# Optimization experiments

Hardware: AMD Instinct MI355X
Metric: run time of the kernel (lower is better)

## Reference

```python
import jax, jax.numpy as jnp
import numpy as np

K = 3  # spatial window (window_size = [1,3,3,1])


def _extract_patches(x, k):
    """TF-style extract_patches, VALID padding, stride 1, rate 1.
    x: [B,H,W,C] -> [B,Ho,Wo,k*k*C] with depth ordering (ki, kj, c)."""
    B, H, W, C = x.shape
    Ho, Wo = H - k + 1, W - k + 1
    cols = [x[:, ki:ki + Ho, kj:kj + Wo, :] for ki in range(k) for kj in range(k)]
    return jnp.concatenate(cols, axis=-1)


def setup_inputs() -> dict:
    key = jax.random.key(0)
    k1, k2 = jax.random.split(key)
    x = jax.random.normal(k1, (8, 32, 32, 32), dtype=jnp.float32)
    # weight shape per build(): (1, 1, 1, K*K*C, filters) = (1,1,1,288,64)
    w = jax.random.normal(k2, (1, 1, 1, 3 * 3 * 32, 64), dtype=jnp.float32) * 0.05
    bias = jnp.zeros((64,), dtype=jnp.float32)
    return {"x": x, "w": w, "bias": bias}


def reference(x, w, bias):
    # patches: [B,Ho,Wo,KKC]
    p = _extract_patches(x, K)
    # broadcast add: [B,Ho,Wo,KKC,1] + [KKC,F] -> [B,Ho,Wo,KKC,F]
    r = p[..., None] + w[0, 0, 0]
    # tropical conv: max-plus minus min-plus over the patch axis, plus bias
    return jnp.max(r, axis=3) - jnp.min(r, axis=3) + bias
```

## Files before the change

kernel.cpp:

```cpp
#include <hip/hip_runtime.h>
#include <math.h>


#define NCOL 10

__global__ __launch_bounds__(256) void trop_kernel(
    const float* __restrict__ x, const float* __restrict__ w,
    const float* __restrict__ bias, float* __restrict__ out) {
  __shared__ float wl[96 * 64];
  __shared__ float xt[3 * 32 * NCOL];

  const int jg = blockIdx.x;
  const int i = blockIdx.y;
  const int b = blockIdx.z;
  const int tid = threadIdx.x;
  const int f = tid & 63;
  const int wave = tid >> 6;
  const int jw = wave * 2;
  const int j0 = jg * 8;

  const float* xb = x + (((size_t)b * 32 + i) * 32) * 32;
  if (tid < 240) {
    int ki = tid / 80;
    int rem = tid % 80;
    int col = rem / 8;
    int c4 = (rem % 8) * 4;
    if (j0 + col < 32) {
      float4 v = *(const float4*)(xb + ((size_t)(ki * 32 + j0 + col)) * 32 + c4);
      xt[(ki * 32 + c4 + 0) * NCOL + col] = v.x;
      xt[(ki * 32 + c4 + 1) * NCOL + col] = v.y;
      xt[(ki * 32 + c4 + 2) * NCOL + col] = v.z;
      xt[(ki * 32 + c4 + 3) * NCOL + col] = v.w;
    }
  }

  float mx0 = -INFINITY, mx1 = -INFINITY;
  float mn0 = INFINITY, mn1 = INFINITY;

  for (int ki = 0; ki < 3; ++ki) {
    __syncthreads();
    const float4* wg = (const float4*)(w + ki * 96 * 64);
    float4* wld = (float4*)wl;
#pragma unroll
    for (int t = 0; t < 6; ++t) wld[tid + t * 256] = wg[tid + t * 256];
    __syncthreads();

#pragma unroll
    for (int c = 0; c < 32; ++c) {
      const float* row = &xt[(ki * 32 + c) * NCOL];
      float2 a = *(const float2*)(row + jw);
      float2 d = *(const float2*)(row + jw + 2);
      float w0 = wl[(0 * 32 + c) * 64 + f];
      float w1 = wl[(1 * 32 + c) * 64 + f];
      float w2 = wl[(2 * 32 + c) * 64 + f];
      float t00 = a.x + w0, t01 = a.y + w0;
      float t10 = a.y + w1, t11 = d.x + w1;
      float t20 = d.x + w2, t21 = d.y + w2;
      mx0 = fmaxf(mx0, fmaxf(t00, fmaxf(t10, t20)));
      mx1 = fmaxf(mx1, fmaxf(t01, fmaxf(t11, t21)));
      mn0 = fminf(mn0, fminf(t00, fminf(t10, t20)));
      mn1 = fminf(mn1, fminf(t01, fminf(t11, t21)));
    }
  }

  float bv = bias[f];
  float* ob = out + (((size_t)b * 30 + i) * 30) * 64 + f;
  int j = j0 + jw;
  if (j < 30) ob[(size_t)j * 64] = mx0 - mn0 + bv;
  if (j + 1 < 30) ob[(size_t)(j + 1) * 64] = mx1 - mn1 + bv;
}

extern "C" void kernel_launch(void* const* d_in, const int* in_sizes, int n_in,
                              void* d_out, int out_size, void* d_ws, size_t ws_size,
                              hipStream_t stream) {
  const float* x = (const float*)d_in[0];
  const float* w = (const float*)d_in[1];
  const float* bias = (const float*)d_in[2];
  float* out = (float*)d_out;
  dim3 grid(4, 30, 8);
  dim3 block(256);
  hipLaunchKernelGGL(trop_kernel, grid, block, 0, stream, x, w, bias, out);
}
```

Baseline: 71.78 us.

## Compute four output columns per thread with direct wave-uniform input loads

Drops the LDS staging of the input tile and has each wave read its six input columns straight from global memory. The column offset is made wave-uniform with readfirstlane, so those loads can become scalar loads. Each thread now produces four output columns instead of two, and the grid's column dimension shrinks from 4 to 2 blocks. Each shared-memory weight element is therefore reused over more outputs, and the total weight staging traffic is halved. The two column groups overlap at columns 14-15, which are computed and written twice with identical values; fewer blocks also means less parallelism.

```diff
diff --git a/kernel.cpp b/kernel.cpp
--- a/kernel.cpp
+++ b/kernel.cpp
@@ -1,41 +1,22 @@
 #include <hip/hip_runtime.h>
 #include <math.h>
 
-
-#define NCOL 10
 
 __global__ __launch_bounds__(256) void trop_kernel(
     const float* __restrict__ x, const float* __restrict__ w,
     const float* __restrict__ bias, float* __restrict__ out) {
   __shared__ float wl[96 * 64];
-  __shared__ float xt[3 * 32 * NCOL];
 
   const int jg = blockIdx.x;
   const int i = blockIdx.y;
   const int b = blockIdx.z;
   const int tid = threadIdx.x;
   const int f = tid & 63;
-  const int wave = tid >> 6;
-  const int jw = wave * 2;
-  const int j0 = jg * 8;
+  const int jwu = __builtin_amdgcn_readfirstlane(tid >> 6) * 4;
+  const int j0 = jg * 14 + jwu;
 
-  const float* xb = x + (((size_t)b * 32 + i) * 32) * 32;
-  if (tid < 240) {
-    int ki = tid / 80;
-    int rem = tid % 80;
-    int col = rem / 8;
-    int c4 = (rem % 8) * 4;
-    if (j0 + col < 32) {
-      float4 v = *(const float4*)(xb + ((size_t)(ki * 32 + j0 + col)) * 32 + c4);
-      xt[(ki * 32 + c4 + 0) * NCOL + col] = v.x;
-      xt[(ki * 32 + c4 + 1) * NCOL + col] = v.y;
-      xt[(ki * 32 + c4 + 2) * NCOL + col] = v.z;
-      xt[(ki * 32 + c4 + 3) * NCOL + col] = v.w;
-    }
-  }
-
-  float mx0 = -INFINITY, mx1 = -INFINITY;
-  float mn0 = INFINITY, mn1 = INFINITY;
+  float mx[4] = {-INFINITY, -INFINITY, -INFINITY, -INFINITY};
+  float mn[4] = {INFINITY, INFINITY, INFINITY, INFINITY};
 
   for (int ki = 0; ki < 3; ++ki) {
     __syncthreads();
@@ -45,29 +26,42 @@
     for (int t = 0; t < 6; ++t) wld[tid + t * 256] = wg[tid + t * 256];
     __syncthreads();
 
+    const float* xr = x + (((size_t)b * 32 + (i + ki)) * 32 + j0) * 32;
+
 #pragma unroll
-    for (int c = 0; c < 32; ++c) {
-      const float* row = &xt[(ki * 32 + c) * NCOL];
-      float2 a = *(const float2*)(row + jw);
-      float2 d = *(const float2*)(row + jw + 2);
-      float w0 = wl[(0 * 32 + c) * 64 + f];
-      float w1 = wl[(1 * 32 + c) * 64 + f];
-      float w2 = wl[(2 * 32 + c) * 64 + f];
-      float t00 = a.x + w0, t01 = a.y + w0;
-      float t10 = a.y + w1, t11 = d.x + w1;
-      float t20 = d.x + w2, t21 = d.y + w2;
-      mx0 = fmaxf(mx0, fmaxf(t00, fmaxf(t10, t20)));
-      mx1 = fmaxf(mx1, fmaxf(t01, fmaxf(t11, t21)));
-      mn0 = fminf(mn0, fminf(t00, fminf(t10, t20)));
-      mn1 = fminf(mn1, fminf(t01, fminf(t11, t21)));
+    for (int c8 = 0; c8 < 32; c8 += 8) {
+      float4 xa[6][2];
+#pragma unroll
+      for (int col = 0; col < 6; ++col) {
+        xa[col][0] = *(const float4*)(xr + col * 32 + c8);
+        xa[col][1] = *(const float4*)(xr + col * 32 + c8 + 4);
+      }
+      const float* wbase = &wl[c8 * 64 + f];
+#pragma unroll
+      for (int c = 0; c < 8; ++c) {
+        float w0 = wbase[c * 64];
+        float w1 = wbase[32 * 64 + c * 64];
+        float w2 = wbase[64 * 64 + c * 64];
+        float xv[6];
+#pragma unroll
+        for (int col = 0; col < 6; ++col)
+          xv[col] = ((const float*)xa[col])[c];
+#pragma unroll
+        for (int p = 0; p < 4; ++p) {
+          float a0 = xv[p + 0] + w0;
+          float a1 = xv[p + 1] + w1;
+          float a2 = xv[p + 2] + w2;
+          mx[p] = fmaxf(mx[p], fmaxf(a0, fmaxf(a1, a2)));
+          mn[p] = fminf(mn[p], fminf(a0, fminf(a1, a2)));
+        }
+      }
     }
   }
 
   float bv = bias[f];
-  float* ob = out + (((size_t)b * 30 + i) * 30) * 64 + f;
-  int j = j0 + jw;
-  if (j < 30) ob[(size_t)j * 64] = mx0 - mn0 + bv;
-  if (j + 1 < 30) ob[(size_t)(j + 1) * 64] = mx1 - mn1 + bv;
+  float* ob = out + (((size_t)b * 30 + i) * 30 + j0) * 64 + f;
+#pragma unroll
+  for (int p = 0; p < 4; ++p) ob[p * 64] = mx[p] - mn[p] + bv;
 }
 
 extern "C" void kernel_launch(void* const* d_in, const int* in_sizes, int n_in,
@@ -77,7 +71,7 @@
   const float* w = (const float*)d_in[1];
   const float* bias = (const float*)d_in[2];
   float* out = (float*)d_out;
-  dim3 grid(4, 30, 8);
+  dim3 grid(2, 30, 8);
   dim3 block(256);
   hipLaunchKernelGGL(trop_kernel, grid, block, 0, stream, x, w, bias, out);
 }
```

New measurement: 69.60 us. 1.03x faster.
